# Kernel optimization log

Measured on AMD Instinct MI355X. Metric: run time of the kernel, lower is better.

## Reference

```python
import jax, jax.numpy as jnp
import numpy as np

DIM = 1024
N_HEADS = 16
HEAD_DIM = DIM // N_HEADS


def setup_inputs() -> dict:
    key = jax.random.key(0)
    k_x, k_qkv, k_out = jax.random.split(key, 3)
    B, L = 4, 2048
    x = jax.random.normal(k_x, (B, L, DIM), dtype=jnp.float32)
    # torch Linear weight has shape [out, in]; y = x @ W.T
    s = 1.0 / np.sqrt(DIM)
    W_qkv = jax.random.uniform(k_qkv, (3 * DIM, DIM), dtype=jnp.float32, minval=-s, maxval=s)
    W_out = jax.random.uniform(k_out, (DIM, DIM), dtype=jnp.float32, minval=-s, maxval=s)
    return {"x": x, "W_qkv": W_qkv, "W_out": W_out}


def reference(x, W_qkv, W_out):
    B, L, D = x.shape
    H, Hd = N_HEADS, HEAD_DIM
    scale = Hd ** (-0.5)
    qkv = x @ W_qkv.T                       # [B, L, 3D]
    q, k, v = jnp.split(qkv, 3, axis=-1)
    # 'b l (h d) -> b h l d'
    q = q.reshape(B, L, H, Hd).transpose(0, 2, 1, 3)
    k = k.reshape(B, L, H, Hd).transpose(0, 2, 1, 3)
    v = v.reshape(B, L, H, Hd).transpose(0, 2, 1, 3)
    attn = jnp.einsum('bhld,bhmd->bhlm', q, k) * scale  # [B, H, L, L]
    causal = jnp.tril(jnp.ones((L, L), dtype=bool))
    attn = jnp.where(causal, attn, -jnp.inf)
    attn = jax.nn.softmax(attn, axis=-1)
    out = jnp.einsum('bhlm,bhmd->bhld', attn, v)        # [B, H, L, Hd]
    out = out.transpose(0, 2, 1, 3).reshape(B, L, D)    # 'b h l d -> b l (h d)'
    return out @ W_out.T
```

## Files before the change

### kernel.cpp

```cpp
#include <hip/hip_runtime.h>
#include <stdint.h>

#define BATCH 4
#define SEQ   2048
#define DIM_  1024
#define NHEAD 16
#define HDIM  64

#define QSC 0.18033688011112042f

typedef __attribute__((ext_vector_type(8)))  short bf8;
typedef __attribute__((ext_vector_type(4)))  short s4v;
typedef __attribute__((ext_vector_type(4)))  float f4;
typedef __attribute__((ext_vector_type(16))) float f16v;
typedef __attribute__((ext_vector_type(2)))  unsigned int u2;
typedef __attribute__((ext_vector_type(4)))  unsigned int u4;

#define MFMA(a, b, c)   __builtin_amdgcn_mfma_f32_16x16x32_bf16(a, b, c, 0, 0, 0)
#define MFMA32(a, b, c) __builtin_amdgcn_mfma_f32_32x32x16_bf16(a, b, c, 0, 0, 0)

#define BAR_LGKM() asm volatile("s_waitcnt lgkmcnt(0)\n\ts_barrier" ::: "memory")

static __device__ __forceinline__ short f2b(float f) {
    uint32_t u = __builtin_bit_cast(uint32_t, f);
    u = (u + 0x7FFFu + ((u >> 16) & 1u)) >> 16;
    return (short)u;
}

static __device__ __forceinline__ uint32_t cvtpk(float lo, float hi) {
    uint32_t r;
    asm("v_cvt_pk_bf16_f32 %0, %1, %2" : "=v"(r) : "v"(lo), "v"(hi));
    return r;
}

typedef const uint32_t __attribute__((address_space(1)))* gas_t;
typedef uint32_t __attribute__((address_space(3)))* las_t;
static __device__ __forceinline__ void gl_lds16(const short* g, short* l) {
    __builtin_amdgcn_global_load_lds((gas_t)g, (las_t)l, 16, 0, 0);
}

__global__ void cvt_all(const float* __restrict__ x, const float* __restrict__ wq,
                        const float* __restrict__ wo, short* __restrict__ xb,
                        short* __restrict__ wqb, short* __restrict__ wob) {
    const int NX = BATCH * SEQ * DIM_ / 4, NQ = 3 * DIM_ * DIM_ / 4;
    int i = blockIdx.x * blockDim.x + threadIdx.x;
    const float4* in; s4v* out; int j;
    if (i < NX)           { in = (const float4*)x;  out = (s4v*)xb;  j = i; }
    else if (i < NX + NQ) { in = (const float4*)wq; out = (s4v*)wqb; j = i - NX; }
    else                  { in = (const float4*)wo; out = (s4v*)wob; j = i - NX - NQ; }
    float4 v = in[j];
    s4v o;
    o.x = f2b(v.x); o.y = f2b(v.y); o.z = f2b(v.z); o.w = f2b(v.w);
    out[j] = o;
}

#define GEMM_PROLOG()                                                         \
    __shared__ __align__(16) short As[128 * 32];                              \
    __shared__ __align__(16) short Bs[128 * 32];                              \
    const int tid  = threadIdx.x;                                             \
    const int lane = tid & 63;                                                \
    const int wave = tid >> 6;                                                \
    const int quad = lane >> 4, l16 = lane & 15;                              \
    const int wr = wave >> 1, wc = wave & 1;                                  \
    const int m0 = blockIdx.y * 128;                                          \
    const int n0 = blockIdx.x * 128;                                          \
    const int srow = tid >> 2;                                                \
    const int sx   = ((tid & 3) ^ ((tid >> 3) & 3)) * 8;    \
    const short* Ag0 = A + (size_t)(m0 + srow) * 1024 + sx;                   \
    const short* Ag1 = Ag0 + (size_t)64 * 1024;                               \
    const short* Bg0 = W + (size_t)(n0 + srow) * 1024 + sx;                   \
    const short* Bg1 = Bg0 + (size_t)64 * 1024;                               \
    short* Al0 = As + tid * 8;                     \
    short* Al1 = Al0 + 64 * 32;                                               \
    short* Bl0 = Bs + tid * 8;                                                \
    short* Bl1 = Bl0 + 64 * 32;                                               \
    const int akey = (l16 >> 1) & 3;                                          \
    const short* afp = As + (wr * 64 + l16) * 32 + (quad ^ akey) * 8;         \
    const short* bfp = Bs + (wc * 64 + l16) * 32 + (quad ^ akey) * 8;         \
    f4 acc[4][4] = {};

#define GEMM_KLOOP()                                                          \
    for (int k0 = 0; k0 < 1024; k0 += 32) {                                   \
        __syncthreads();                                                      \
        gl_lds16(Ag0 + k0, Al0);                                              \
        gl_lds16(Ag1 + k0, Al1);                                              \
        gl_lds16(Bg0 + k0, Bl0);                                              \
        gl_lds16(Bg1 + k0, Bl1);                                              \
        __syncthreads();                                                      \
        bf8 a[4], b[4];                                                       \
        _Pragma("unroll") for (int i = 0; i < 4; ++i) {                       \
            a[i] = *(const bf8*)(afp + i * 16 * 32);                          \
            b[i] = *(const bf8*)(bfp + i * 16 * 32);                          \
        }                                                                     \
        _Pragma("unroll") for (int mt = 0; mt < 4; ++mt)                      \
            _Pragma("unroll") for (int nt = 0; nt < 4; ++nt)                  \
                acc[mt][nt] = MFMA(a[mt], b[nt], acc[mt][nt]);                \
    }

__global__ __launch_bounds__(256) void gemm_qkv(const short* __restrict__ A,
                                                const short* __restrict__ W,
                                                short* __restrict__ Qd,
                                                short* __restrict__ Kd,
                                                short* __restrict__ Vd) {
    GEMM_PROLOG();
    GEMM_KLOOP();

    short* const bases[3] = {Qd, Kd, Vd};
    #pragma unroll
    for (int mt = 0; mt < 4; ++mt) {
        const int row = m0 + wr * 64 + mt * 16 + quad * 4;
        #pragma unroll
        for (int nt = 0; nt < 4; ++nt) {
            const int colb  = n0 + wc * 64 + nt * 16;
            const int which = colb >> 10;
            const int hh    = (colb >> 6) & 15;
            const int d0    = colb & 63;
            const float sc_ = (which == 0) ? QSC : 1.0f;
            short* bp = bases[which];
            #pragma unroll
            for (int r = 0; r < 4; ++r) {
                const int t  = row + r;
                const int bb = t >> 11, ll = t & 2047;
                bp[((size_t)(bb * NHEAD + hh) * SEQ + ll) * 64 + d0 + l16] =
                    f2b(acc[mt][nt][r] * sc_);
            }
        }
    }
}

__global__ __launch_bounds__(256) void gemm_bt(const short* __restrict__ A,
                                               const short* __restrict__ W,
                                               float* __restrict__ Cp) {
    GEMM_PROLOG();
    GEMM_KLOOP();

    #pragma unroll
    for (int mt = 0; mt < 4; ++mt) {
        const int row = m0 + wr * 64 + mt * 16 + quad * 4;
        #pragma unroll
        for (int nt = 0; nt < 4; ++nt) {
            const int col = n0 + wc * 64 + nt * 16 + l16;
            #pragma unroll
            for (int r = 0; r < 4; ++r)
                Cp[(size_t)(row + r) * DIM_ + col] = acc[mt][nt][r];
        }
    }
}

__global__ __launch_bounds__(256) void flash_attn(const short* __restrict__ Qd,
                                                  const short* __restrict__ Kd,
                                                  const short* __restrict__ Vd,
                                                  short* __restrict__ out) {
    const int bh = blockIdx.x;
    const int b  = bh >> 4, h = bh & 15;
    const int qt = (gridDim.y - 1) - blockIdx.y;
    const int q0 = qt * 128;
    const int tid  = threadIdx.x;
    const int lane = tid & 63, wave = tid >> 6;
    const int l32  = lane & 31, khalf = lane >> 5;

    __shared__ __align__(16) short Ks[64 * 72];
    __shared__ __align__(16) short Vt[64 * 72];
    uint32_t* Vt32 = (uint32_t*)Vt;

    const short* Qp = Qd + (size_t)bh * (SEQ * 64);
    const short* Kp = Kd + (size_t)bh * (SEQ * 64);
    const short* Vp = Vd + (size_t)bh * (SEQ * 64);

    const int qrow = q0 + wave * 32 + l32;
    bf8 qf[4];
    #pragma unroll
    for (int dk = 0; dk < 4; ++dk)
        qf[dk] = *(const bf8*)(Qp + (size_t)qrow * 64 + dk * 16 + khalf * 8);

    const int skey = tid >> 2, sc = tid & 3;
    const int vkp = tid & 31, vds = (tid >> 5) * 8;

    bf8 ka0 = *(const bf8*)(Kp + (size_t)skey * 64 + sc * 8);
    bf8 ka1 = *(const bf8*)(Kp + (size_t)skey * 64 + (sc + 4) * 8);
    bf8 vr0 = *(const bf8*)(Vp + (size_t)(2 * vkp) * 64 + vds);
    bf8 vr1 = *(const bf8*)(Vp + (size_t)(2 * vkp + 1) * 64 + vds);

    f16v o0 = {}, o1 = {};
    float lsum = 0.f;
    const bf8 zz = {};

    const int nIter = 2 * qt + 2;
    for (int it = 0; it < nIter; ++it) {
        const int k0 = it * 64;

        BAR_LGKM();
        *(bf8*)(&Ks[skey * 72 + sc * 8])       = ka0;
        *(bf8*)(&Ks[skey * 72 + (sc + 4) * 8]) = ka1;
        #pragma unroll
        for (int i = 0; i < 8; ++i) {
            uint32_t p = (uint32_t)(uint16_t)vr0[i] | ((uint32_t)(uint16_t)vr1[i] << 16);
            Vt32[(vds + i) * 36 + vkp] = p;
        }
        BAR_LGKM();

        if (it + 1 < nIter) {
            const int kn = k0 + 64;
            ka0 = *(const bf8*)(Kp + (size_t)(kn + skey) * 64 + sc * 8);
            ka1 = *(const bf8*)(Kp + (size_t)(kn + skey) * 64 + (sc + 4) * 8);
            vr0 = *(const bf8*)(Vp + (size_t)(kn + 2 * vkp) * 64 + vds);
            vr1 = *(const bf8*)(Vp + (size_t)(kn + 2 * vkp + 1) * 64 + vds);
        }

        if (q0 + wave * 32 < k0) continue;

        bf8 pf[4];
        #pragma unroll
        for (int kt = 0; kt < 2; ++kt) {
            const int ktbase = k0 + kt * 32;
            const int rel = (q0 + wave * 32) - ktbase;
            if (rel < 0) {
                pf[kt * 2] = zz; pf[kt * 2 + 1] = zz;
                continue;
            }
            f16v st = {};
            __builtin_amdgcn_s_setprio(1);
            #pragma unroll
            for (int dk = 0; dk < 4; ++dk) {
                bf8 kf = *(const bf8*)(&Ks[(kt * 32 + l32) * 72 + dk * 16 + khalf * 8]);
                st = MFMA32(kf, qf[dk], st);
            }
            __builtin_amdgcn_s_setprio(0);
            float P[16];
            if (rel == 0) {
                #pragma unroll
                for (int r = 0; r < 16; ++r) {
                    const int kg = ktbase + (r & 3) + 8 * (r >> 2) + 4 * khalf;
                    float pv = __builtin_amdgcn_exp2f(st[r]);
                    P[r] = (kg > qrow) ? 0.0f : pv;
                }
            } else {
                #pragma unroll
                for (int r = 0; r < 16; ++r) P[r] = __builtin_amdgcn_exp2f(st[r]);
            }
            uint32_t w0 = cvtpk(P[0],  P[1]),  w1 = cvtpk(P[2],  P[3]);
            uint32_t w2 = cvtpk(P[4],  P[5]),  w3 = cvtpk(P[6],  P[7]);
            uint32_t w4 = cvtpk(P[8],  P[9]),  w5 = cvtpk(P[10], P[11]);
            uint32_t w6 = cvtpk(P[12], P[13]), w7 = cvtpk(P[14], P[15]);
            u2 s02 = __builtin_amdgcn_permlane32_swap(w0, w2, false, false);
            u2 s13 = __builtin_amdgcn_permlane32_swap(w1, w3, false, false);
            u2 s46 = __builtin_amdgcn_permlane32_swap(w4, w6, false, false);
            u2 s57 = __builtin_amdgcn_permlane32_swap(w5, w7, false, false);
            u4 q0w = {s02[0], s13[0], s02[1], s13[1]};
            u4 q1w = {s46[0], s57[0], s46[1], s57[1]};
            pf[kt * 2]     = __builtin_bit_cast(bf8, q0w);
            pf[kt * 2 + 1] = __builtin_bit_cast(bf8, q1w);
            float ls = ((P[0] + P[1]) + (P[2] + P[3])) +
                       ((P[4] + P[5]) + (P[6] + P[7])) +
                       ((P[8] + P[9]) + (P[10] + P[11])) +
                       ((P[12] + P[13]) + (P[14] + P[15]));
            lsum += ls;
        }

        __builtin_amdgcn_s_setprio(1);
        #pragma unroll
        for (int ks = 0; ks < 4; ++ks) {
            bf8 v0 = *(const bf8*)(&Vt[(l32) * 72 + ks * 16 + khalf * 8]);
            bf8 v1 = *(const bf8*)(&Vt[(32 + l32) * 72 + ks * 16 + khalf * 8]);
            o0 = MFMA32(pf[ks], v0, o0);
            o1 = MFMA32(pf[ks], v1, o1);
        }
        __builtin_amdgcn_s_setprio(0);
    }

    lsum += __shfl_xor(lsum, 32);
    short* outp = out + ((size_t)(b * SEQ + q0 + wave * 32) * DIM_) + h * 64;
    #pragma unroll
    for (int r = 0; r < 16; ++r) {
        const int rowl = (r & 3) + 8 * (r >> 2) + 4 * khalf;
        const float inv = 1.0f / __shfl(lsum, rowl);
        outp[(size_t)rowl * DIM_ + l32]      = f2b(o0[r] * inv);
        outp[(size_t)rowl * DIM_ + 32 + l32] = f2b(o1[r] * inv);
    }
}

extern "C" void kernel_launch(void* const* d_in, const int* in_sizes, int n_in,
                              void* d_out, int out_size, void* d_ws, size_t ws_size,
                              hipStream_t stream) {
    const float* x    = (const float*)d_in[0];
    const float* wqkv = (const float*)d_in[1];
    const float* wout = (const float*)d_in[2];

    char* ws = (char*)d_ws;
    short* xb    = (short*)(ws);
    short* wqkvb = (short*)(ws + (size_t)(16) * (1 << 20));
    short* woutb = (short*)(ws + (size_t)(22) * (1 << 20));
    short* Qd    = (short*)(ws + (size_t)(24) * (1 << 20));
    short* Kd    = (short*)(ws + (size_t)(40) * (1 << 20));
    short* Vd    = (short*)(ws + (size_t)(56) * (1 << 20));
    short* attnb = (short*)(ws + (size_t)(72) * (1 << 20));

    const int ntot = (BATCH * SEQ * DIM_ + 3 * DIM_ * DIM_ + DIM_ * DIM_) / 4;
    cvt_all<<<(ntot + 255) / 256, 256, 0, stream>>>(x, wqkv, wout, xb, wqkvb, woutb);

    gemm_qkv<<<dim3(3 * DIM_ / 128, BATCH * SEQ / 128), 256, 0, stream>>>(
        xb, wqkvb, Qd, Kd, Vd);

    flash_attn<<<dim3(BATCH * NHEAD, SEQ / 128), 256, 0, stream>>>(Qd, Kd, Vd, attnb);

    gemm_bt<<<dim3(DIM_ / 128, BATCH * SEQ / 128), 256, 0, stream>>>(
        attnb, woutb, (float*)d_out);
}
```

Before: 235.0 us.

## Triple-buffer GEMM k-loop with 256x128 tiles and split async LDS prefetch

Replaces the single-buffered 128x128, K=32 GEMM loop used by the QKV and output projections with a 256x128 tile, 512-thread, K=64 loop. The loop rotates three LDS buffers so direct global-to-LDS loads for future k-steps overlap MFMA work, with explicit vmcnt waits and raw barriers in place of two full syncs per step. Each k-step is split into two halves that interleave part of the prefetch, and wave priority is raised around the MFMA blocks. This aims to hide global load latency and cut barrier stalls, but roughly 144KB of LDS per block limits occupancy to one block per CU and halves the grid size.

```diff
diff --git a/kernel.cpp b/kernel.cpp
--- a/kernel.cpp
+++ b/kernel.cpp
@@ -20,6 +20,7 @@
 #define MFMA32(a, b, c) __builtin_amdgcn_mfma_f32_32x32x16_bf16(a, b, c, 0, 0, 0)
 
 #define BAR_LGKM() asm volatile("s_waitcnt lgkmcnt(0)\n\ts_barrier" ::: "memory")
+#define PBAR() asm volatile("s_barrier" ::: "memory")
 
 static __device__ __forceinline__ short f2b(float f) {
     uint32_t u = __builtin_bit_cast(uint32_t, f);
@@ -54,56 +55,105 @@
     out[j] = o;
 }
 
-#define GEMM_PROLOG()                                                         \
-    __shared__ __align__(16) short As[128 * 32];                              \
-    __shared__ __align__(16) short Bs[128 * 32];                              \
+#define LDSB 24576
+#define NT   16
+
+#define PG_PROLOG()                                                           \
+    __shared__ __align__(16) short lds[3 * LDSB];                             \
     const int tid  = threadIdx.x;                                             \
     const int lane = tid & 63;                                                \
     const int wave = tid >> 6;                                                \
     const int quad = lane >> 4, l16 = lane & 15;                              \
     const int wr = wave >> 1, wc = wave & 1;                                  \
-    const int m0 = blockIdx.y * 128;                                          \
+    const int m0 = blockIdx.y * 256;                                          \
     const int n0 = blockIdx.x * 128;                                          \
-    const int srow = tid >> 2;                                                \
-    const int sx   = ((tid & 3) ^ ((tid >> 3) & 3)) * 8;    \
-    const short* Ag0 = A + (size_t)(m0 + srow) * 1024 + sx;                   \
-    const short* Ag1 = Ag0 + (size_t)64 * 1024;                               \
-    const short* Bg0 = W + (size_t)(n0 + srow) * 1024 + sx;                   \
-    const short* Bg1 = Bg0 + (size_t)64 * 1024;                               \
-    short* Al0 = As + tid * 8;                     \
-    short* Al1 = Al0 + 64 * 32;                                               \
-    short* Bl0 = Bs + tid * 8;                                                \
-    short* Bl1 = Bl0 + 64 * 32;                                               \
-    const int akey = (l16 >> 1) & 3;                                          \
-    const short* afp = As + (wr * 64 + l16) * 32 + (quad ^ akey) * 8;         \
-    const short* bfp = Bs + (wc * 64 + l16) * 32 + (quad ^ akey) * 8;         \
+    \
+    const short* gA[4]; int dA[4];                                            \
+    _Pragma("unroll") for (int j = 0; j < 4; ++j) {                           \
+        const int idx = j * 512 + tid;                                        \
+        const int row = idx >> 3, pos = idx & 7;                              \
+        gA[j] = A + (size_t)(m0 + row) * 1024 + (pos ^ (row & 7)) * 8;        \
+        dA[j] = idx * 8;                                                      \
+    }                                                                         \
+    const short* gB[2]; int dB[2];                                            \
+    _Pragma("unroll") for (int j = 0; j < 2; ++j) {                           \
+        const int idx = j * 512 + tid;                                        \
+        const int row = idx >> 3, pos = idx & 7;                              \
+        gB[j] = W + (size_t)(n0 + row) * 1024 + (pos ^ (row & 7)) * 8;        \
+        dB[j] = 16384 + idx * 8;                                              \
+    }                                                                         \
+                       \
+    int aro[4], bro[4];                                                       \
+    _Pragma("unroll") for (int i = 0; i < 4; ++i) {                           \
+        aro[i] = (wr * 64 + i * 16 + l16) * 64;                               \
+        bro[i] = 16384 + (wc * 64 + i * 16 + l16) * 64;                       \
+    }                                                                         \
+    const int kx = l16 & 7;                                                   \
+    short* cur = lds; short* nxt = lds + LDSB; short* stg = lds + 2 * LDSB;   \
     f4 acc[4][4] = {};
 
-#define GEMM_KLOOP()                                                          \
-    for (int k0 = 0; k0 < 1024; k0 += 32) {                                   \
-        __syncthreads();                                                      \
-        gl_lds16(Ag0 + k0, Al0);                                              \
-        gl_lds16(Ag1 + k0, Al1);                                              \
-        gl_lds16(Bg0 + k0, Bl0);                                              \
-        gl_lds16(Bg1 + k0, Bl1);                                              \
-        __syncthreads();                                                      \
+#define PG_STAGE6(bp)                                                         \
+    do {                                                                      \
+        gl_lds16(gA[0], (bp) + dA[0]); gl_lds16(gA[1], (bp) + dA[1]);         \
+        gl_lds16(gA[2], (bp) + dA[2]); gl_lds16(gA[3], (bp) + dA[3]);         \
+        gl_lds16(gB[0], (bp) + dB[0]); gl_lds16(gB[1], (bp) + dB[1]);         \
+        _Pragma("unroll") for (int j = 0; j < 4; ++j) gA[j] += 64;            \
+        gB[0] += 64; gB[1] += 64;                                             \
+    } while (0)
+
+#define PG_KLOOP()                                                            \
+    PG_STAGE6(cur);                                               \
+    PG_STAGE6(nxt);                                               \
+    asm volatile("s_waitcnt vmcnt(6)\n\ts_barrier" ::: "memory");             \
+    for (int t = 0; t < NT; ++t) {                                            \
+        const bool pre = (t < NT - 2);                                        \
         bf8 a[4], b[4];                                                       \
+                                              \
         _Pragma("unroll") for (int i = 0; i < 4; ++i) {                       \
-            a[i] = *(const bf8*)(afp + i * 16 * 32);                          \
-            b[i] = *(const bf8*)(bfp + i * 16 * 32);                          \
+            a[i] = *(const bf8*)(cur + aro[i] + ((0 + quad) ^ kx) * 8);       \
+            b[i] = *(const bf8*)(cur + bro[i] + ((0 + quad) ^ kx) * 8);       \
         }                                                                     \
+        if (pre) {                                                            \
+            gl_lds16(gA[0], stg + dA[0]); gl_lds16(gA[1], stg + dA[1]);       \
+            gl_lds16(gA[2], stg + dA[2]);                                     \
+        }                                                                     \
+        PBAR();                                                               \
+        __builtin_amdgcn_s_setprio(1);                                        \
         _Pragma("unroll") for (int mt = 0; mt < 4; ++mt)                      \
             _Pragma("unroll") for (int nt = 0; nt < 4; ++nt)                  \
                 acc[mt][nt] = MFMA(a[mt], b[nt], acc[mt][nt]);                \
-    }
-
-__global__ __launch_bounds__(256) void gemm_qkv(const short* __restrict__ A,
-                                                const short* __restrict__ W,
-                                                short* __restrict__ Qd,
-                                                short* __restrict__ Kd,
-                                                short* __restrict__ Vd) {
-    GEMM_PROLOG();
-    GEMM_KLOOP();
+        __builtin_amdgcn_s_setprio(0);                                        \
+        PBAR();                                                               \
+                                              \
+        _Pragma("unroll") for (int i = 0; i < 4; ++i) {                       \
+            a[i] = *(const bf8*)(cur + aro[i] + ((4 + quad) ^ kx) * 8);       \
+            b[i] = *(const bf8*)(cur + bro[i] + ((4 + quad) ^ kx) * 8);       \
+        }                                                                     \
+        if (pre) {                                                            \
+            gl_lds16(gA[3], stg + dA[3]);                                     \
+            gl_lds16(gB[0], stg + dB[0]); gl_lds16(gB[1], stg + dB[1]);       \
+            _Pragma("unroll") for (int j = 0; j < 4; ++j) gA[j] += 64;        \
+            gB[0] += 64; gB[1] += 64;                                         \
+        }                                                                     \
+        PBAR();                                                               \
+        __builtin_amdgcn_s_setprio(1);                                        \
+        _Pragma("unroll") for (int mt = 0; mt < 4; ++mt)                      \
+            _Pragma("unroll") for (int nt = 0; nt < 4; ++nt)                  \
+                acc[mt][nt] = MFMA(a[mt], b[nt], acc[mt][nt]);                \
+        __builtin_amdgcn_s_setprio(0);                                        \
+         \
+        if (pre) asm volatile("s_waitcnt vmcnt(6)\n\ts_barrier" ::: "memory");\
+        else     asm volatile("s_waitcnt vmcnt(0)\n\ts_barrier" ::: "memory");\
+        short* tmp = cur; cur = nxt; nxt = stg; stg = tmp;                    \
+    }
+
+__global__ __launch_bounds__(512, 2) void gemm_qkv(const short* __restrict__ A,
+                                                   const short* __restrict__ W,
+                                                   short* __restrict__ Qd,
+                                                   short* __restrict__ Kd,
+                                                   short* __restrict__ Vd) {
+    PG_PROLOG();
+    PG_KLOOP();
 
     short* const bases[3] = {Qd, Kd, Vd};
     #pragma unroll
@@ -128,11 +178,11 @@
     }
 }
 
-__global__ __launch_bounds__(256) void gemm_bt(const short* __restrict__ A,
-                                               const short* __restrict__ W,
-                                               float* __restrict__ Cp) {
-    GEMM_PROLOG();
-    GEMM_KLOOP();
+__global__ __launch_bounds__(512, 2) void gemm_bt(const short* __restrict__ A,
+                                                  const short* __restrict__ W,
+                                                  float* __restrict__ Cp) {
+    PG_PROLOG();
+    PG_KLOOP();
 
     #pragma unroll
     for (int mt = 0; mt < 4; ++mt) {
@@ -298,11 +348,11 @@
     const int ntot = (BATCH * SEQ * DIM_ + 3 * DIM_ * DIM_ + DIM_ * DIM_) / 4;
     cvt_all<<<(ntot + 255) / 256, 256, 0, stream>>>(x, wqkv, wout, xb, wqkvb, woutb);
 
-    gemm_qkv<<<dim3(3 * DIM_ / 128, BATCH * SEQ / 128), 256, 0, stream>>>(
+    gemm_qkv<<<dim3(3 * DIM_ / 128, BATCH * SEQ / 256), 512, 0, stream>>>(
         xb, wqkvb, Qd, Kd, Vd);
 
     flash_attn<<<dim3(BATCH * NHEAD, SEQ / 128), 256, 0, stream>>>(Qd, Kd, Vd, attnb);
 
-    gemm_bt<<<dim3(DIM_ / 128, BATCH * SEQ / 128), 256, 0, stream>>>(
+    gemm_bt<<<dim3(DIM_ / 128, BATCH * SEQ / 256), 512, 0, stream>>>(
         attnb, woutb, (float*)d_out);
 }
```

Result: no change. 232.4 us (-1.1%).

## Triple-buffer GEMM K-loop with async global-to-LDS prefetch two stages ahead

Applied to the files above, without the earlier changes.

Replaces the single-buffered GEMM K-loop, which had two barriers per step, with a three-buffer rotating LDS pipeline that issues global_load_lds for tile t+2 while computing tile t. Each step uses a single vmcnt wait plus barrier. MFMA priority is raised with s_setprio, and both GEMMs get launch_bounds with 3 blocks per CU. The intent is to hide global load latency behind MFMA work. The cost is 48KB of LDS per block, which may limit occupancy.

```diff
diff --git a/kernel.cpp b/kernel.cpp
--- a/kernel.cpp
+++ b/kernel.cpp
@@ -54,9 +54,11 @@
     out[j] = o;
 }
 
-#define GEMM_PROLOG()                                                         \
-    __shared__ __align__(16) short As[128 * 32];                              \
-    __shared__ __align__(16) short Bs[128 * 32];                              \
+#define NT2  32
+#define BUF2 8192
+
+#define PG_PROLOG()                                                           \
+    __shared__ __align__(16) short lds[3 * BUF2];                             \
     const int tid  = threadIdx.x;                                             \
     const int lane = tid & 63;                                                \
     const int wave = tid >> 6;                                                \
@@ -70,40 +72,56 @@
     const short* Ag1 = Ag0 + (size_t)64 * 1024;                               \
     const short* Bg0 = W + (size_t)(n0 + srow) * 1024 + sx;                   \
     const short* Bg1 = Bg0 + (size_t)64 * 1024;                               \
-    short* Al0 = As + tid * 8;                     \
-    short* Al1 = Al0 + 64 * 32;                                               \
-    short* Bl0 = Bs + tid * 8;                                                \
-    short* Bl1 = Bl0 + 64 * 32;                                               \
+    const int dA0 = tid * 8,        dA1 = 2048 + tid * 8;                     \
+    const int dB0 = 4096 + tid * 8, dB1 = 6144 + tid * 8;                     \
     const int akey = (l16 >> 1) & 3;                                          \
-    const short* afp = As + (wr * 64 + l16) * 32 + (quad ^ akey) * 8;         \
-    const short* bfp = Bs + (wc * 64 + l16) * 32 + (quad ^ akey) * 8;         \
+    const int aoff = (wr * 64 + l16) * 32 + (quad ^ akey) * 8;                \
+    const int boff = 4096 + (wc * 64 + l16) * 32 + (quad ^ akey) * 8;         \
     f4 acc[4][4] = {};
 
-#define GEMM_KLOOP()                                                          \
-    for (int k0 = 0; k0 < 1024; k0 += 32) {                                   \
-        __syncthreads();                                                      \
-        gl_lds16(Ag0 + k0, Al0);                                              \
-        gl_lds16(Ag1 + k0, Al1);                                              \
-        gl_lds16(Bg0 + k0, Bl0);                                              \
-        gl_lds16(Bg1 + k0, Bl1);                                              \
-        __syncthreads();                                                      \
-        bf8 a[4], b[4];                                                       \
-        _Pragma("unroll") for (int i = 0; i < 4; ++i) {                       \
-            a[i] = *(const bf8*)(afp + i * 16 * 32);                          \
-            b[i] = *(const bf8*)(bfp + i * 16 * 32);                          \
+#define PG_STAGE(bp, tt)                                                      \
+    do {                                                                      \
+        const int ko = (tt) * 32;                                             \
+        gl_lds16(Ag0 + ko, (bp) + dA0);                                       \
+        gl_lds16(Ag1 + ko, (bp) + dA1);                                       \
+        gl_lds16(Bg0 + ko, (bp) + dB0);                                       \
+        gl_lds16(Bg1 + ko, (bp) + dB1);                                       \
+    } while (0)
+
+#define PG_KLOOP()                                                            \
+    {                                                                         \
+        short* cur = lds; short* nxt = lds + BUF2; short* stg = lds + 2 * BUF2;\
+        PG_STAGE(cur, 0);                                                     \
+        PG_STAGE(nxt, 1);                                                     \
+        asm volatile("s_waitcnt vmcnt(4)\n\ts_barrier" ::: "memory");         \
+        for (int t = 0; t < NT2; ++t) {                                       \
+            bf8 a[4], b[4];                                                   \
+            _Pragma("unroll") for (int i = 0; i < 4; ++i) {                   \
+                a[i] = *(const bf8*)(cur + aoff + i * 512);                   \
+                b[i] = *(const bf8*)(cur + boff + i * 512);                   \
+            }                                                                 \
+            if (t < NT2 - 2) PG_STAGE(stg, t + 2);                            \
+            __builtin_amdgcn_s_setprio(1);                                    \
+            _Pragma("unroll") for (int mt = 0; mt < 4; ++mt)                  \
+                _Pragma("unroll") for (int nt = 0; nt < 4; ++nt)              \
+                    acc[mt][nt] = MFMA(a[mt], b[nt], acc[mt][nt]);            \
+            __builtin_amdgcn_s_setprio(0);                                    \
+                 \
+            if (t < NT2 - 2)                                                  \
+                asm volatile("s_waitcnt vmcnt(4)\n\ts_barrier" ::: "memory"); \
+            else                                                              \
+                asm volatile("s_waitcnt vmcnt(0)\n\ts_barrier" ::: "memory"); \
+            short* tmp = cur; cur = nxt; nxt = stg; stg = tmp;                \
         }                                                                     \
-        _Pragma("unroll") for (int mt = 0; mt < 4; ++mt)                      \
-            _Pragma("unroll") for (int nt = 0; nt < 4; ++nt)                  \
-                acc[mt][nt] = MFMA(a[mt], b[nt], acc[mt][nt]);                \
-    }
-
-__global__ __launch_bounds__(256) void gemm_qkv(const short* __restrict__ A,
-                                                const short* __restrict__ W,
-                                                short* __restrict__ Qd,
-                                                short* __restrict__ Kd,
-                                                short* __restrict__ Vd) {
-    GEMM_PROLOG();
-    GEMM_KLOOP();
+    }
+
+__global__ __launch_bounds__(256, 3) void gemm_qkv(const short* __restrict__ A,
+                                                   const short* __restrict__ W,
+                                                   short* __restrict__ Qd,
+                                                   short* __restrict__ Kd,
+                                                   short* __restrict__ Vd) {
+    PG_PROLOG();
+    PG_KLOOP();
 
     short* const bases[3] = {Qd, Kd, Vd};
     #pragma unroll
@@ -128,11 +146,11 @@
     }
 }
 
-__global__ __launch_bounds__(256) void gemm_bt(const short* __restrict__ A,
-                                               const short* __restrict__ W,
-                                               float* __restrict__ Cp) {
-    GEMM_PROLOG();
-    GEMM_KLOOP();
+__global__ __launch_bounds__(256, 3) void gemm_bt(const short* __restrict__ A,
+                                                  const short* __restrict__ W,
+                                                  float* __restrict__ Cp) {
+    PG_PROLOG();
+    PG_KLOOP();
 
     #pragma unroll
     for (int mt = 0; mt < 4; ++mt) {
```

New measurement: 227.6 us. -3.2%, faster.

## Fuse fp32-to-bf16 conversion into GEMM loads with double-buffered LDS pipeline

Applied to the files above, without the earlier changes.

Removes the separate conversion kernel. Both GEMMs now read fp32 inputs and weights directly through registers, pack them to bf16 and write them into a double-buffered LDS tile, prefetching two k-steps ahead. MFMA sections get a raised wave priority, and launch bounds request 3 waves per SIMD. This drops a full extra pass over x and the weights, but the GEMMs now load twice as many bytes in fp32 and redo the weight conversion in every block instead of using the direct global-to-LDS loads.

```diff
diff --git a/kernel.cpp b/kernel.cpp
--- a/kernel.cpp
+++ b/kernel.cpp
@@ -10,7 +10,6 @@
 #define QSC 0.18033688011112042f
 
 typedef __attribute__((ext_vector_type(8)))  short bf8;
-typedef __attribute__((ext_vector_type(4)))  short s4v;
 typedef __attribute__((ext_vector_type(4)))  float f4;
 typedef __attribute__((ext_vector_type(16))) float f16v;
 typedef __attribute__((ext_vector_type(2)))  unsigned int u2;
@@ -33,30 +32,11 @@
     return r;
 }
 
-typedef const uint32_t __attribute__((address_space(1)))* gas_t;
-typedef uint32_t __attribute__((address_space(3)))* las_t;
-static __device__ __forceinline__ void gl_lds16(const short* g, short* l) {
-    __builtin_amdgcn_global_load_lds((gas_t)g, (las_t)l, 16, 0, 0);
-}
-
-__global__ void cvt_all(const float* __restrict__ x, const float* __restrict__ wq,
-                        const float* __restrict__ wo, short* __restrict__ xb,
-                        short* __restrict__ wqb, short* __restrict__ wob) {
-    const int NX = BATCH * SEQ * DIM_ / 4, NQ = 3 * DIM_ * DIM_ / 4;
-    int i = blockIdx.x * blockDim.x + threadIdx.x;
-    const float4* in; s4v* out; int j;
-    if (i < NX)           { in = (const float4*)x;  out = (s4v*)xb;  j = i; }
-    else if (i < NX + NQ) { in = (const float4*)wq; out = (s4v*)wqb; j = i - NX; }
-    else                  { in = (const float4*)wo; out = (s4v*)wob; j = i - NX - NQ; }
-    float4 v = in[j];
-    s4v o;
-    o.x = f2b(v.x); o.y = f2b(v.y); o.z = f2b(v.z); o.w = f2b(v.w);
-    out[j] = o;
-}
-
-#define GEMM_PROLOG()                                                         \
-    __shared__ __align__(16) short As[128 * 32];                              \
-    __shared__ __align__(16) short Bs[128 * 32];                              \
+#define NT2  32
+#define BUF2 8192
+
+#define GEO_PROLOG()                                                          \
+    __shared__ __align__(16) short lds[2 * BUF2];                             \
     const int tid  = threadIdx.x;                                             \
     const int lane = tid & 63;                                                \
     const int wave = tid >> 6;                                                \
@@ -66,44 +46,66 @@
     const int n0 = blockIdx.x * 128;                                          \
     const int srow = tid >> 2;                                                \
     const int sx   = ((tid & 3) ^ ((tid >> 3) & 3)) * 8;    \
-    const short* Ag0 = A + (size_t)(m0 + srow) * 1024 + sx;                   \
-    const short* Ag1 = Ag0 + (size_t)64 * 1024;                               \
-    const short* Bg0 = W + (size_t)(n0 + srow) * 1024 + sx;                   \
-    const short* Bg1 = Bg0 + (size_t)64 * 1024;                               \
-    short* Al0 = As + tid * 8;                     \
-    short* Al1 = Al0 + 64 * 32;                                               \
-    short* Bl0 = Bs + tid * 8;                                                \
-    short* Bl1 = Bl0 + 64 * 32;                                               \
+    const int dA0 = tid * 8,        dA1 = 2048 + tid * 8;                     \
+    const int dB0 = 4096 + tid * 8, dB1 = 6144 + tid * 8;                     \
     const int akey = (l16 >> 1) & 3;                                          \
-    const short* afp = As + (wr * 64 + l16) * 32 + (quad ^ akey) * 8;         \
-    const short* bfp = Bs + (wc * 64 + l16) * 32 + (quad ^ akey) * 8;         \
+    const int aoff = (wr * 64 + l16) * 32 + (quad ^ akey) * 8;                \
+    const int boff = 4096 + (wc * 64 + l16) * 32 + (quad ^ akey) * 8;         \
     f4 acc[4][4] = {};
 
-#define GEMM_KLOOP()                                                          \
-    for (int k0 = 0; k0 < 1024; k0 += 32) {                                   \
-        __syncthreads();                                                      \
-        gl_lds16(Ag0 + k0, Al0);                                              \
-        gl_lds16(Ag1 + k0, Al1);                                              \
-        gl_lds16(Bg0 + k0, Bl0);                                              \
-        gl_lds16(Bg1 + k0, Bl1);                                              \
-        __syncthreads();                                                      \
-        bf8 a[4], b[4];                                                       \
-        _Pragma("unroll") for (int i = 0; i < 4; ++i) {                       \
-            a[i] = *(const bf8*)(afp + i * 16 * 32);                          \
-            b[i] = *(const bf8*)(bfp + i * 16 * 32);                          \
-        }                                                                     \
-        _Pragma("unroll") for (int mt = 0; mt < 4; ++mt)                      \
-            _Pragma("unroll") for (int nt = 0; nt < 4; ++nt)                  \
-                acc[mt][nt] = MFMA(a[mt], b[nt], acc[mt][nt]);                \
-    }
-
-__global__ __launch_bounds__(256) void gemm_qkv(const short* __restrict__ A,
-                                                const short* __restrict__ W,
-                                                short* __restrict__ Qd,
-                                                short* __restrict__ Kd,
-                                                short* __restrict__ Vd) {
-    GEMM_PROLOG();
-    GEMM_KLOOP();
+#define PK8(v0, v1) (u4){cvtpk(v0.x, v0.y), cvtpk(v0.z, v0.w),                \
+                         cvtpk(v1.x, v1.y), cvtpk(v1.z, v1.w)}
+
+#define GEMM_FRAGS_MFMA()                                                     \
+    bf8 a[4], b[4];                                                           \
+    _Pragma("unroll") for (int i = 0; i < 4; ++i) {                           \
+        a[i] = *(const bf8*)(cur + aoff + i * 512);                           \
+        b[i] = *(const bf8*)(cur + boff + i * 512);                           \
+    }
+
+#define GEMM_MFMA16()                                                         \
+    __builtin_amdgcn_s_setprio(1);                                            \
+    _Pragma("unroll") for (int mt = 0; mt < 4; ++mt)                          \
+        _Pragma("unroll") for (int nt = 0; nt < 4; ++nt)                      \
+            acc[mt][nt] = MFMA(a[mt], b[nt], acc[mt][nt]);                    \
+    __builtin_amdgcn_s_setprio(0);
+
+__global__ __launch_bounds__(256, 3) void gemm_qkv(const float* __restrict__ X,
+                                                   const float* __restrict__ Wq,
+                                                   short* __restrict__ Qd,
+                                                   short* __restrict__ Kd,
+                                                   short* __restrict__ Vd) {
+    GEO_PROLOG();
+    const float* Ax0 = X  + (size_t)(m0 + srow) * 1024 + sx;
+    const float* Ax1 = Ax0 + (size_t)64 * 1024;
+    const float* Bw0 = Wq + (size_t)(n0 + srow) * 1024 + sx;
+    const float* Bw1 = Bw0 + (size_t)64 * 1024;
+    float4 la0, la1, la2, la3, lb0, lb1, lb2, lb3;
+
+#define QLD(ko)                                                               \
+    la0 = *(const float4*)(Ax0 + (ko)); la1 = *(const float4*)(Ax0 + (ko) + 4);\
+    la2 = *(const float4*)(Ax1 + (ko)); la3 = *(const float4*)(Ax1 + (ko) + 4);\
+    lb0 = *(const float4*)(Bw0 + (ko)); lb1 = *(const float4*)(Bw0 + (ko) + 4);\
+    lb2 = *(const float4*)(Bw1 + (ko)); lb3 = *(const float4*)(Bw1 + (ko) + 4);
+#define QWR(bp)                                                               \
+    *(u4*)((bp) + dA0) = PK8(la0, la1);                                       \
+    *(u4*)((bp) + dA1) = PK8(la2, la3);                                       \
+    *(u4*)((bp) + dB0) = PK8(lb0, lb1);                                       \
+    *(u4*)((bp) + dB1) = PK8(lb2, lb3);
+
+    short* cur = lds; short* oth = lds + BUF2;
+    QLD(0); QWR(cur); QLD(32);
+    BAR_LGKM();
+    for (int t = 0; t < NT2; ++t) {
+        GEMM_FRAGS_MFMA();
+        if (t + 1 < NT2) { QWR(oth); }
+        if (t + 2 < NT2) { QLD((t + 2) * 32); }
+        GEMM_MFMA16();
+        BAR_LGKM();
+        short* tmp = cur; cur = oth; oth = tmp;
+    }
+#undef QLD
+#undef QWR
 
     short* const bases[3] = {Qd, Kd, Vd};
     #pragma unroll
@@ -128,11 +130,41 @@
     }
 }
 
-__global__ __launch_bounds__(256) void gemm_bt(const short* __restrict__ A,
-                                               const short* __restrict__ W,
-                                               float* __restrict__ Cp) {
-    GEMM_PROLOG();
-    GEMM_KLOOP();
+__global__ __launch_bounds__(256, 3) void gemm_bt(const short* __restrict__ Ab,
+                                                  const float* __restrict__ Wo,
+                                                  float* __restrict__ Cp) {
+    GEO_PROLOG();
+    const short* Aa0 = Ab + (size_t)(m0 + srow) * 1024 + sx;
+    const short* Aa1 = Aa0 + (size_t)64 * 1024;
+    const float* Bw0 = Wo + (size_t)(n0 + srow) * 1024 + sx;
+    const float* Bw1 = Bw0 + (size_t)64 * 1024;
+    u4 ra0, ra1;
+    float4 lb0, lb1, lb2, lb3;
+
+#define TLD(ko)                                                               \
+    ra0 = *(const u4*)(Aa0 + (ko));                                           \
+    ra1 = *(const u4*)(Aa1 + (ko));                                           \
+    lb0 = *(const float4*)(Bw0 + (ko)); lb1 = *(const float4*)(Bw0 + (ko) + 4);\
+    lb2 = *(const float4*)(Bw1 + (ko)); lb3 = *(const float4*)(Bw1 + (ko) + 4);
+#define TWR(bp)                                                               \
+    *(u4*)((bp) + dA0) = ra0;                                                 \
+    *(u4*)((bp) + dA1) = ra1;                                                 \
+    *(u4*)((bp) + dB0) = PK8(lb0, lb1);                                       \
+    *(u4*)((bp) + dB1) = PK8(lb2, lb3);
+
+    short* cur = lds; short* oth = lds + BUF2;
+    TLD(0); TWR(cur); TLD(32);
+    BAR_LGKM();
+    for (int t = 0; t < NT2; ++t) {
+        GEMM_FRAGS_MFMA();
+        if (t + 1 < NT2) { TWR(oth); }
+        if (t + 2 < NT2) { TLD((t + 2) * 32); }
+        GEMM_MFMA16();
+        BAR_LGKM();
+        short* tmp = cur; cur = oth; oth = tmp;
+    }
+#undef TLD
+#undef TWR
 
     #pragma unroll
     for (int mt = 0; mt < 4; ++mt) {
@@ -287,22 +319,16 @@
     const float* wout = (const float*)d_in[2];
 
     char* ws = (char*)d_ws;
-    short* xb    = (short*)(ws);
-    short* wqkvb = (short*)(ws + (size_t)(16) * (1 << 20));
-    short* woutb = (short*)(ws + (size_t)(22) * (1 << 20));
-    short* Qd    = (short*)(ws + (size_t)(24) * (1 << 20));
-    short* Kd    = (short*)(ws + (size_t)(40) * (1 << 20));
-    short* Vd    = (short*)(ws + (size_t)(56) * (1 << 20));
-    short* attnb = (short*)(ws + (size_t)(72) * (1 << 20));
-
-    const int ntot = (BATCH * SEQ * DIM_ + 3 * DIM_ * DIM_ + DIM_ * DIM_) / 4;
-    cvt_all<<<(ntot + 255) / 256, 256, 0, stream>>>(x, wqkv, wout, xb, wqkvb, woutb);
+    short* Qd    = (short*)(ws);
+    short* Kd    = (short*)(ws + (size_t)(16) * (1 << 20));
+    short* Vd    = (short*)(ws + (size_t)(32) * (1 << 20));
+    short* attnb = (short*)(ws + (size_t)(48) * (1 << 20));
 
     gemm_qkv<<<dim3(3 * DIM_ / 128, BATCH * SEQ / 128), 256, 0, stream>>>(
-        xb, wqkvb, Qd, Kd, Vd);
+        x, wqkv, Qd, Kd, Vd);
 
     flash_attn<<<dim3(BATCH * NHEAD, SEQ / 128), 256, 0, stream>>>(Qd, Kd, Vd, attnb);
 
     gemm_bt<<<dim3(DIM_ / 128, BATCH * SEQ / 128), 256, 0, stream>>>(
-        attnb, woutb, (float*)d_out);
-}
+        attnb, wout, (float*)d_out);
+}
```

New measurement: 256.6 us. 9.2% more time.
